# Kernel optimization log

Measured on AMD Instinct MI355X. Metric: run time of the kernel, lower is better.

Reference implementation:

```python
import jax, jax.numpy as jnp
import numpy as np

NUM_GRAPHS = 512  # number of segments (graphs) in the batch
NEG_SLOPE = 0.01  # nn.LeakyReLU default


def setup_inputs() -> dict:
    key = jax.random.key(0)
    k1, k2, k3, k4, k5 = jax.random.split(key, 5)
    N, D = 200000, 128
    h_topo = jax.random.normal(k1, (N, D), dtype=jnp.float32)
    h_geom = jax.random.normal(k2, (N, D), dtype=jnp.float32)
    batch = jnp.sort(jax.random.randint(k3, (N,), 0, NUM_GRAPHS, dtype=jnp.int64))
    concat_dim, hidden, out_dim = 6 * D, 2 * D, 128
    W1 = jax.random.normal(k4, (concat_dim, hidden), dtype=jnp.float32) * 0.02
    b1 = jnp.zeros((hidden,), dtype=jnp.float32)
    W2 = jax.random.normal(k5, (hidden, out_dim), dtype=jnp.float32) * 0.02
    b2 = jnp.zeros((out_dim,), dtype=jnp.float32)
    return {"h_topo": h_topo, "h_geom": h_geom, "batch": batch,
            "W1": W1, "b1": b1, "W2": W2, "b2": b2}


def _pool_feats(h, batch):
    # global_max_pool / global_mean_pool keyed by graph id, gathered back per node
    gmax = jax.ops.segment_max(h, batch, num_segments=NUM_GRAPHS)
    gsum = jax.ops.segment_sum(h, batch, num_segments=NUM_GRAPHS)
    cnt = jax.ops.segment_sum(jnp.ones((h.shape[0],), h.dtype), batch,
                              num_segments=NUM_GRAPHS)
    gmean = gsum / jnp.maximum(cnt, 1.0)[:, None]
    return gmax[batch], gmean[batch]  # [N, D] each


def reference(h_topo, h_geom, batch, W1, b1, W2, b2):
    t_max, t_mean = _pool_feats(h_topo, batch)
    g_max, g_mean = _pool_feats(h_geom, batch)
    # [Topo, Geom, TopoMax, TopoMean, GeomMax, GeomMean]
    combined = jnp.concatenate(
        [h_topo, t_max, t_mean, h_geom, g_max, g_mean], axis=-1)  # [N, 6D]
    h = combined @ W1 + b1
    h = jnp.where(h >= 0, h, NEG_SLOPE * h)  # LeakyReLU
    return h @ W2 + b2
```

## Files before the change

### kernel.cpp

```cpp
#include <hip/hip_runtime.h>
#include <math.h>

#define NUM_GRAPHS 512
#define D 128
#define NEG 0.01f
#define BN 64

typedef __attribute__((ext_vector_type(8))) short  bf16x8;
typedef __attribute__((ext_vector_type(4))) float  f32x4;

__device__ __forceinline__ unsigned short f2bf(float f) {
    unsigned u = __float_as_uint(f);
    u += 0x7fffu + ((u >> 16) & 1u);
    return (unsigned short)(u >> 16);
}

__device__ __forceinline__ uint2 pack4(float4 v) {
    uint2 pk;
    pk.x = (unsigned)f2bf(v.x) | ((unsigned)f2bf(v.y) << 16);
    pk.y = (unsigned)f2bf(v.z) | ((unsigned)f2bf(v.w) << 16);
    return pk;
}

__device__ __forceinline__ int swz(int row, int k) {
    return row * 256 + (k ^ ((row & 7) << 3));
}

#define GLD16(gsrc, ldst)                                                    \
    __builtin_amdgcn_global_load_lds(                                        \
        (const __attribute__((address_space(1))) void*)(gsrc),               \
        (__attribute__((address_space(3))) void*)(ldst), 16, 0, 0)

#define LDS_BARRIER()                                                        \
    do {                                                                     \
        asm volatile("s_waitcnt lgkmcnt(0)" ::: "memory");                   \
        __builtin_amdgcn_s_barrier();                                        \
        asm volatile("" ::: "memory");                                       \
    } while (0)

__global__ __launch_bounds__(256) void pool_kernel(
    const float* __restrict__ h_topo, const float* __restrict__ h_geom,
    const int* __restrict__ batch, int N, float* __restrict__ pooled,
    unsigned short* __restrict__ xt)
{
    const int g = blockIdx.x, t = blockIdx.y;
    const float* __restrict__ h = t ? h_geom : h_topo;
    const int koff = t ? 128 : 0;

    int lo = 0, hi = N;
    while (lo < hi) { int m = (lo + hi) >> 1; if (batch[m] < g) lo = m + 1; else hi = m; }
    const int start = lo; hi = N;
    while (lo < hi) { int m = (lo + hi) >> 1; if (batch[m] < g + 1) lo = m + 1; else hi = m; }
    const int end = lo;

    const int c = threadIdx.x & 31;
    const int r = threadIdx.x >> 5;
    const int kk = koff + c * 4;

    float4 mx  = make_float4(-INFINITY, -INFINITY, -INFINITY, -INFINITY);
    float4 mx2 = mx;
    float4 sm  = make_float4(0.f, 0.f, 0.f, 0.f);
    float4 sm2 = sm;

    int row = start + r;
    for (; row + 8 < end; row += 16) {
        float4 v = *(const float4*)(h + (size_t)row * D + c * 4);
        float4 w = *(const float4*)(h + (size_t)(row + 8) * D + c * 4);
        mx.x  = fmaxf(mx.x,  v.x); mx.y  = fmaxf(mx.y,  v.y);
        mx.z  = fmaxf(mx.z,  v.z); mx.w  = fmaxf(mx.w,  v.w);
        sm.x += v.x; sm.y += v.y; sm.z += v.z; sm.w += v.w;
        mx2.x = fmaxf(mx2.x, w.x); mx2.y = fmaxf(mx2.y, w.y);
        mx2.z = fmaxf(mx2.z, w.z); mx2.w = fmaxf(mx2.w, w.w);
        sm2.x += w.x; sm2.y += w.y; sm2.z += w.z; sm2.w += w.w;
        *(uint2*)(xt + (size_t)(row >> 6) * 16384 + swz(row & 63, kk)) = pack4(v);
        *(uint2*)(xt + (size_t)((row + 8) >> 6) * 16384 + swz((row + 8) & 63, kk)) = pack4(w);
    }
    if (row < end) {
        float4 v = *(const float4*)(h + (size_t)row * D + c * 4);
        mx.x  = fmaxf(mx.x,  v.x); mx.y  = fmaxf(mx.y,  v.y);
        mx.z  = fmaxf(mx.z,  v.z); mx.w  = fmaxf(mx.w,  v.w);
        sm.x += v.x; sm.y += v.y; sm.z += v.z; sm.w += v.w;
        *(uint2*)(xt + (size_t)(row >> 6) * 16384 + swz(row & 63, kk)) = pack4(v);
    }
    mx.x = fmaxf(mx.x, mx2.x); mx.y = fmaxf(mx.y, mx2.y);
    mx.z = fmaxf(mx.z, mx2.z); mx.w = fmaxf(mx.w, mx2.w);
    sm.x += sm2.x; sm.y += sm2.y; sm.z += sm2.z; sm.w += sm2.w;

    __shared__ float4 smx[256], ssm[256];
    smx[threadIdx.x] = mx; ssm[threadIdx.x] = sm;
    __syncthreads();
    #pragma unroll
    for (int s = 4; s > 0; s >>= 1) {
        if (r < s) {
            float4 a = smx[threadIdx.x + s * 32];
            float4 b = ssm[threadIdx.x + s * 32];
            float4 m0 = smx[threadIdx.x];
            float4 s0 = ssm[threadIdx.x];
            m0.x = fmaxf(m0.x, a.x); m0.y = fmaxf(m0.y, a.y);
            m0.z = fmaxf(m0.z, a.z); m0.w = fmaxf(m0.w, a.w);
            s0.x += b.x; s0.y += b.y; s0.z += b.z; s0.w += b.w;
            smx[threadIdx.x] = m0; ssm[threadIdx.x] = s0;
        }
        __syncthreads();
    }
    if (r == 0) {
        float4 m0 = smx[threadIdx.x], s0 = ssm[threadIdx.x];
        const float inv = 1.0f / fmaxf((float)(end - start), 1.0f);
        float4 mean = make_float4(s0.x * inv, s0.y * inv, s0.z * inv, s0.w * inv);
        if (end <= start) { m0 = make_float4(0,0,0,0); mean = make_float4(0,0,0,0); }
        float* dst = pooled + (size_t)g * 512 + t * 256;
        *(float4*)(dst + c * 4)       = m0;
        *(float4*)(dst + 128 + c * 4) = mean;
    }
}

__global__ __launch_bounds__(256) void pmat_kernel(
    const float* __restrict__ pooled, const float* __restrict__ W1,
    const float* __restrict__ b1, float* __restrict__ P)
{
    const int g = blockIdx.x;
    const int j = threadIdx.x;

    __shared__ float pl[512];
    pl[j]       = pooled[(size_t)g * 512 + j];
    pl[j + 256] = pooled[(size_t)g * 512 + 256 + j];
    __syncthreads();

    float acc = b1[j];
    #pragma unroll 8
    for (int k = 0; k < 256; ++k)
        acc += pl[k] * W1[(size_t)(128 + k) * 256 + j];
    #pragma unroll 8
    for (int k = 0; k < 256; ++k)
        acc += pl[256 + k] * W1[(size_t)(512 + k) * 256 + j];

    P[(size_t)g * 256 + j] = acc;
}

__global__ __launch_bounds__(256) void wconv_kernel(
    const float* __restrict__ W1, const float* __restrict__ W2,
    unsigned short* __restrict__ W1bT, unsigned short* __restrict__ W2bT)
{
    const int idx = blockIdx.x * 256 + threadIdx.x;
    if (idx < 256 * 256) {
        const int n = idx >> 8, k = idx & 255;
        const int kk = (k < 128) ? k : (k + 256);
        W1bT[idx] = f2bf(W1[(size_t)kk * 256 + n]);
    } else {
        const int j = idx - 256 * 256;
        if (j < 128 * 256) {
            const int n = j >> 8, k = j & 255;
            W2bT[j] = f2bf(W2[(size_t)k * 128 + n]);
        }
    }
}

__global__ __launch_bounds__(256, 3) void mlp_mfma(
    const unsigned short* __restrict__ xt, const int* __restrict__ batch,
    const float* __restrict__ P,
    const unsigned short* __restrict__ W1bT, const unsigned short* __restrict__ W2bT,
    const float* __restrict__ b2, float* __restrict__ out, int N)
{
    __shared__ unsigned short xs[64 * 256];
    __shared__ int gid[64];

    const int tid  = threadIdx.x;
    const int wave = tid >> 6, lane = tid & 63;
    const int base = blockIdx.x * BN;
    const size_t tbase = (size_t)blockIdx.x * 16384;

    #pragma unroll
    for (int c = 0; c < 8; ++c) {
        const int off = wave * 4096 + c * 512;
        GLD16(xt + tbase + off + lane * 8, xs + off);
    }
    if (tid < 64) gid[tid] = batch[min(base + tid, N - 1)];

    const int g0 = batch[base];
    const int g1 = batch[min(base + 63, N - 1)];
    const bool uni = (g0 == g1);

    const int lhi = lane >> 4;
    const int llo = lane & 15;

    const unsigned short* w1p = W1bT + (size_t)(wave * 64 + llo) * 256 + lhi * 8;
    const unsigned short* w2p = W2bT + (size_t)(wave * 32 + llo) * 256 + lhi * 8;

    float pf[4];
    if (uni) {
        #pragma unroll
        for (int ct = 0; ct < 4; ++ct)
            pf[ct] = P[(size_t)g0 * 256 + wave * 64 + ct * 16 + llo];
    }

    bf16x8 bfr[2][4];
    #pragma unroll
    for (int ct = 0; ct < 4; ++ct)
        bfr[0][ct] = *(const bf16x8*)(w1p + (size_t)ct * 16 * 256);

    asm volatile("s_waitcnt vmcnt(0)" ::: "memory");
    __syncthreads();

    f32x4 acc[4][4];
    #pragma unroll
    for (int rt = 0; rt < 4; ++rt)
        #pragma unroll
        for (int ct = 0; ct < 4; ++ct) {
            const float p = uni ? pf[ct] : 0.f;
            acc[rt][ct] = (f32x4){p, p, p, p};
        }

    #pragma unroll
    for (int ks = 0; ks < 8; ++ks) {
        if (ks < 7) {
            const int kbn = (ks + 1) * 32;
            #pragma unroll
            for (int ct = 0; ct < 4; ++ct)
                bfr[(ks + 1) & 1][ct] = *(const bf16x8*)(w1p + (size_t)ct * 16 * 256 + kbn);
        }
        const int kb = ks * 32 + lhi * 8;
        bf16x8 afr[4];
        #pragma unroll
        for (int rt = 0; rt < 4; ++rt)
            afr[rt] = *(const bf16x8*)&xs[swz(rt * 16 + llo, kb)];
        __builtin_amdgcn_s_setprio(1);
        #pragma unroll
        for (int rt = 0; rt < 4; ++rt)
            #pragma unroll
            for (int ct = 0; ct < 4; ++ct)
                acc[rt][ct] = __builtin_amdgcn_mfma_f32_16x16x32_bf16(
                    afr[rt], bfr[ks & 1][ct], acc[rt][ct], 0, 0, 0);
        __builtin_amdgcn_s_setprio(0);
    }

    bf16x8 bfr2[2][2];
    #pragma unroll
    for (int ct = 0; ct < 2; ++ct)
        bfr2[0][ct] = *(const bf16x8*)(w2p + (size_t)ct * 16 * 256);

    LDS_BARRIER();

    #pragma unroll
    for (int rt = 0; rt < 4; ++rt) {
        #pragma unroll
        for (int ct = 0; ct < 4; ++ct) {
            const int col = wave * 64 + ct * 16 + llo;
            #pragma unroll
            for (int q = 0; q < 4; ++q) {
                const int row = rt * 16 + lhi * 4 + q;
                float v = acc[rt][ct][q];
                if (!uni) v += P[(size_t)gid[row] * 256 + col];
                v = fmaxf(v, NEG * v);
                xs[swz(row, col)] = f2bf(v);
            }
        }
    }

    LDS_BARRIER();

    f32x4 acc2[4][2];
    #pragma unroll
    for (int ct = 0; ct < 2; ++ct) {
        const float bv = b2[wave * 32 + ct * 16 + llo];
        #pragma unroll
        for (int rt = 0; rt < 4; ++rt)
            acc2[rt][ct] = (f32x4){bv, bv, bv, bv};
    }
    #pragma unroll
    for (int ks = 0; ks < 8; ++ks) {
        if (ks < 7) {
            const int kbn = (ks + 1) * 32;
            #pragma unroll
            for (int ct = 0; ct < 2; ++ct)
                bfr2[(ks + 1) & 1][ct] = *(const bf16x8*)(w2p + (size_t)ct * 16 * 256 + kbn);
        }
        const int kb = ks * 32 + lhi * 8;
        bf16x8 afr[4];
        #pragma unroll
        for (int rt = 0; rt < 4; ++rt)
            afr[rt] = *(const bf16x8*)&xs[swz(rt * 16 + llo, kb)];
        __builtin_amdgcn_s_setprio(1);
        #pragma unroll
        for (int rt = 0; rt < 4; ++rt)
            #pragma unroll
            for (int ct = 0; ct < 2; ++ct)
                acc2[rt][ct] = __builtin_amdgcn_mfma_f32_16x16x32_bf16(
                    afr[rt], bfr2[ks & 1][ct], acc2[rt][ct], 0, 0, 0);
        __builtin_amdgcn_s_setprio(0);
    }

    #pragma unroll
    for (int rt = 0; rt < 4; ++rt)
        #pragma unroll
        for (int ct = 0; ct < 2; ++ct)
            #pragma unroll
            for (int q = 0; q < 4; ++q) {
                const int row  = rt * 16 + lhi * 4 + q;
                const int node = base + row;
                if (node < N)
                    out[(size_t)node * 128 + wave * 32 + ct * 16 + llo] = acc2[rt][ct][q];
            }
}

extern "C" void kernel_launch(void* const* d_in, const int* in_sizes, int n_in,
                              void* d_out, int out_size, void* d_ws, size_t ws_size,
                              hipStream_t stream)
{
    const float* h_topo = (const float*)d_in[0];
    const float* h_geom = (const float*)d_in[1];
    const int*   batch  = (const int*)  d_in[2];
    const float* W1     = (const float*)d_in[3];
    const float* b1     = (const float*)d_in[4];
    const float* W2     = (const float*)d_in[5];
    const float* b2     = (const float*)d_in[6];
    float* out = (float*)d_out;

    const int N = in_sizes[0] / D;

    float*          pooled = (float*)d_ws;
    float*          P      = pooled + (size_t)NUM_GRAPHS * 512;
    unsigned short* W1bT   = (unsigned short*)(P + (size_t)NUM_GRAPHS * 256);
    unsigned short* W2bT   = W1bT + 256 * 256;

    const size_t small_bytes = (size_t)(NUM_GRAPHS * 512 + NUM_GRAPHS * 256) * 4
                             + (size_t)(256 * 256 + 128 * 256) * 2;
    const size_t xt_bytes = (size_t)N * 256 * 2;

    unsigned short* xt;
    if (ws_size >= small_bytes + xt_bytes)
        xt = (unsigned short*)((char*)d_ws + small_bytes);
    else
        xt = (unsigned short*)d_out;

    wconv_kernel<<<(256 * 256 + 128 * 256) / 256, 256, 0, stream>>>(W1, W2, W1bT, W2bT);
    pool_kernel<<<dim3(NUM_GRAPHS, 2), 256, 0, stream>>>(h_topo, h_geom, batch, N,
                                                         pooled, xt);
    pmat_kernel<<<NUM_GRAPHS, 256, 0, stream>>>(pooled, W1, b1, P);

    mlp_mfma<<<N / BN, 256, 0, stream>>>(xt, batch, P, W1bT, W2bT, b2, out, N);
}
```

Before: 206.3 us.

## Split per-graph pooling across sub-blocks and deepen weight prefetch in MLP kernel

The pooling kernel now splits each graph's node range into four slices, one block per slice, so the grid grows from 1024 to 4096 blocks and covers the GPU better. Each slice writes a partial max and sum. The pmat kernel recomputes the segment bounds and combines the partials into max and mean. Separately, the MLP kernel prefetches W1 fragments two k-steps ahead and W2 fragments four steps ahead, to hide global load latency, at the cost of more registers.

After: 212.5 us. 1.03x slower.

```diff
diff --git a/kernel.cpp b/kernel.cpp
--- a/kernel.cpp
+++ b/kernel.cpp
@@ -5,6 +5,7 @@
 #define D 128
 #define NEG 0.01f
 #define BN 64
+#define NS 4
 
 typedef __attribute__((ext_vector_type(8))) short  bf16x8;
 typedef __attribute__((ext_vector_type(4))) float  f32x4;
@@ -40,10 +41,10 @@
 
 __global__ __launch_bounds__(256) void pool_kernel(
     const float* __restrict__ h_topo, const float* __restrict__ h_geom,
-    const int* __restrict__ batch, int N, float* __restrict__ pooled,
+    const int* __restrict__ batch, int N, float* __restrict__ pp,
     unsigned short* __restrict__ xt)
 {
-    const int g = blockIdx.x, t = blockIdx.y;
+    const int g = blockIdx.x, t = blockIdx.y, s = blockIdx.z;
     const float* __restrict__ h = t ? h_geom : h_topo;
     const int koff = t ? 128 : 0;
 
@@ -53,6 +54,10 @@
     while (lo < hi) { int m = (lo + hi) >> 1; if (batch[m] < g + 1) lo = m + 1; else hi = m; }
     const int end = lo;
 
+    const int len = end - start;
+    const int r0  = start + (int)(((long long)len * s) / NS);
+    const int r1  = start + (int)(((long long)len * (s + 1)) / NS);
+
     const int c = threadIdx.x & 31;
     const int r = threadIdx.x >> 5;
     const int kk = koff + c * 4;
@@ -62,8 +67,8 @@
     float4 sm  = make_float4(0.f, 0.f, 0.f, 0.f);
     float4 sm2 = sm;
 
-    int row = start + r;
-    for (; row + 8 < end; row += 16) {
+    int row = r0 + r;
+    for (; row + 8 < r1; row += 16) {
         float4 v = *(const float4*)(h + (size_t)row * D + c * 4);
         float4 w = *(const float4*)(h + (size_t)(row + 8) * D + c * 4);
         mx.x  = fmaxf(mx.x,  v.x); mx.y  = fmaxf(mx.y,  v.y);
@@ -75,7 +80,7 @@
         *(uint2*)(xt + (size_t)(row >> 6) * 16384 + swz(row & 63, kk)) = pack4(v);
         *(uint2*)(xt + (size_t)((row + 8) >> 6) * 16384 + swz((row + 8) & 63, kk)) = pack4(w);
     }
-    if (row < end) {
+    if (row < r1) {
         float4 v = *(const float4*)(h + (size_t)row * D + c * 4);
         mx.x  = fmaxf(mx.x,  v.x); mx.y  = fmaxf(mx.y,  v.y);
         mx.z  = fmaxf(mx.z,  v.z); mx.w  = fmaxf(mx.w,  v.w);
@@ -90,10 +95,10 @@
     smx[threadIdx.x] = mx; ssm[threadIdx.x] = sm;
     __syncthreads();
     #pragma unroll
-    for (int s = 4; s > 0; s >>= 1) {
-        if (r < s) {
-            float4 a = smx[threadIdx.x + s * 32];
-            float4 b = ssm[threadIdx.x + s * 32];
+    for (int st = 4; st > 0; st >>= 1) {
+        if (r < st) {
+            float4 a = smx[threadIdx.x + st * 32];
+            float4 b = ssm[threadIdx.x + st * 32];
             float4 m0 = smx[threadIdx.x];
             float4 s0 = ssm[threadIdx.x];
             m0.x = fmaxf(m0.x, a.x); m0.y = fmaxf(m0.y, a.y);
@@ -104,26 +109,41 @@
         __syncthreads();
     }
     if (r == 0) {
-        float4 m0 = smx[threadIdx.x], s0 = ssm[threadIdx.x];
-        const float inv = 1.0f / fmaxf((float)(end - start), 1.0f);
-        float4 mean = make_float4(s0.x * inv, s0.y * inv, s0.z * inv, s0.w * inv);
-        if (end <= start) { m0 = make_float4(0,0,0,0); mean = make_float4(0,0,0,0); }
-        float* dst = pooled + (size_t)g * 512 + t * 256;
-        *(float4*)(dst + c * 4)       = m0;
-        *(float4*)(dst + 128 + c * 4) = mean;
+        float* dst = pp + ((size_t)(g * 2 + t) * NS + s) * 256;
+        *(float4*)(dst + c * 4)       = smx[threadIdx.x];
+        *(float4*)(dst + 128 + c * 4) = ssm[threadIdx.x];
     }
 }
 
 __global__ __launch_bounds__(256) void pmat_kernel(
-    const float* __restrict__ pooled, const float* __restrict__ W1,
-    const float* __restrict__ b1, float* __restrict__ P)
+    const float* __restrict__ pp, const int* __restrict__ batch, int N,
+    const float* __restrict__ W1, const float* __restrict__ b1,
+    float* __restrict__ P)
 {
     const int g = blockIdx.x;
     const int j = threadIdx.x;
 
+    int lo = 0, hi = N;
+    while (lo < hi) { int m = (lo + hi) >> 1; if (batch[m] < g) lo = m + 1; else hi = m; }
+    const int start = lo; hi = N;
+    while (lo < hi) { int m = (lo + hi) >> 1; if (batch[m] < g + 1) lo = m + 1; else hi = m; }
+    const int end = lo;
+    const float inv   = 1.0f / fmaxf((float)(end - start), 1.0f);
+    const bool  empty = (end <= start);
+
     __shared__ float pl[512];
-    pl[j]       = pooled[(size_t)g * 512 + j];
-    pl[j + 256] = pooled[(size_t)g * 512 + 256 + j];
+    #pragma unroll
+    for (int e0 = 0; e0 < 2; ++e0) {
+        const int e = j + e0 * 256;
+        const int t = e >> 8, i = e & 255;
+        const float* q = pp + (size_t)(g * 2 + t) * NS * 256 + i;
+        float v;
+        if (i < 128)
+            v = fmaxf(fmaxf(q[0], q[256]), fmaxf(q[512], q[768]));
+        else
+            v = (q[0] + q[256] + q[512] + q[768]) * inv;
+        pl[e] = empty ? 0.f : v;
+    }
     __syncthreads();
 
     float acc = b1[j];
@@ -195,8 +215,10 @@
 
     bf16x8 bfr[2][4];
     #pragma unroll
-    for (int ct = 0; ct < 4; ++ct)
+    for (int ct = 0; ct < 4; ++ct) {
         bfr[0][ct] = *(const bf16x8*)(w1p + (size_t)ct * 16 * 256);
+        bfr[1][ct] = *(const bf16x8*)(w1p + (size_t)ct * 16 * 256 + 32);
+    }
 
     asm volatile("s_waitcnt vmcnt(0)" ::: "memory");
     __syncthreads();
@@ -212,12 +234,6 @@
 
     #pragma unroll
     for (int ks = 0; ks < 8; ++ks) {
-        if (ks < 7) {
-            const int kbn = (ks + 1) * 32;
-            #pragma unroll
-            for (int ct = 0; ct < 4; ++ct)
-                bfr[(ks + 1) & 1][ct] = *(const bf16x8*)(w1p + (size_t)ct * 16 * 256 + kbn);
-        }
         const int kb = ks * 32 + lhi * 8;
         bf16x8 afr[4];
         #pragma unroll
@@ -231,12 +247,20 @@
                 acc[rt][ct] = __builtin_amdgcn_mfma_f32_16x16x32_bf16(
                     afr[rt], bfr[ks & 1][ct], acc[rt][ct], 0, 0, 0);
         __builtin_amdgcn_s_setprio(0);
-    }
-
-    bf16x8 bfr2[2][2];
-    #pragma unroll
-    for (int ct = 0; ct < 2; ++ct)
-        bfr2[0][ct] = *(const bf16x8*)(w2p + (size_t)ct * 16 * 256);
+        if (ks < 6) {
+            const int kbn = (ks + 2) * 32;
+            #pragma unroll
+            for (int ct = 0; ct < 4; ++ct)
+                bfr[ks & 1][ct] = *(const bf16x8*)(w1p + (size_t)ct * 16 * 256 + kbn);
+        }
+    }
+
+    bf16x8 bfr2[4][2];
+    #pragma unroll
+    for (int k0 = 0; k0 < 4; ++k0)
+        #pragma unroll
+        for (int ct = 0; ct < 2; ++ct)
+            bfr2[k0][ct] = *(const bf16x8*)(w2p + (size_t)ct * 16 * 256 + k0 * 32);
 
     LDS_BARRIER();
 
@@ -268,12 +292,6 @@
     }
     #pragma unroll
     for (int ks = 0; ks < 8; ++ks) {
-        if (ks < 7) {
-            const int kbn = (ks + 1) * 32;
-            #pragma unroll
-            for (int ct = 0; ct < 2; ++ct)
-                bfr2[(ks + 1) & 1][ct] = *(const bf16x8*)(w2p + (size_t)ct * 16 * 256 + kbn);
-        }
         const int kb = ks * 32 + lhi * 8;
         bf16x8 afr[4];
         #pragma unroll
@@ -285,8 +303,14 @@
             #pragma unroll
             for (int ct = 0; ct < 2; ++ct)
                 acc2[rt][ct] = __builtin_amdgcn_mfma_f32_16x16x32_bf16(
-                    afr[rt], bfr2[ks & 1][ct], acc2[rt][ct], 0, 0, 0);
+                    afr[rt], bfr2[ks & 3][ct], acc2[rt][ct], 0, 0, 0);
         __builtin_amdgcn_s_setprio(0);
+        if (ks < 4) {
+            const int kbn = (ks + 4) * 32;
+            #pragma unroll
+            for (int ct = 0; ct < 2; ++ct)
+                bfr2[ks & 3][ct] = *(const bf16x8*)(w2p + (size_t)ct * 16 * 256 + kbn);
+        }
     }
 
     #pragma unroll
@@ -317,12 +341,13 @@
 
     const int N = in_sizes[0] / D;
 
-    float*          pooled = (float*)d_ws;
-    float*          P      = pooled + (size_t)NUM_GRAPHS * 512;
-    unsigned short* W1bT   = (unsigned short*)(P + (size_t)NUM_GRAPHS * 256);
-    unsigned short* W2bT   = W1bT + 256 * 256;
-
-    const size_t small_bytes = (size_t)(NUM_GRAPHS * 512 + NUM_GRAPHS * 256) * 4
+    float*          pp   = (float*)d_ws;
+    float*          P    = pp + (size_t)NUM_GRAPHS * 2 * NS * 256;
+    unsigned short* W1bT = (unsigned short*)(P + (size_t)NUM_GRAPHS * 256);
+    unsigned short* W2bT = W1bT + 256 * 256;
+
+    const size_t small_bytes = (size_t)NUM_GRAPHS * 2 * NS * 256 * 4
+                             + (size_t)NUM_GRAPHS * 256 * 4
                              + (size_t)(256 * 256 + 128 * 256) * 2;
     const size_t xt_bytes = (size_t)N * 256 * 2;
 
@@ -333,9 +358,9 @@
         xt = (unsigned short*)d_out;
 
     wconv_kernel<<<(256 * 256 + 128 * 256) / 256, 256, 0, stream>>>(W1, W2, W1bT, W2bT);
-    pool_kernel<<<dim3(NUM_GRAPHS, 2), 256, 0, stream>>>(h_topo, h_geom, batch, N,
-                                                         pooled, xt);
-    pmat_kernel<<<NUM_GRAPHS, 256, 0, stream>>>(pooled, W1, b1, P);
+    pool_kernel<<<dim3(NUM_GRAPHS, 2, NS), 256, 0, stream>>>(h_topo, h_geom, batch, N,
+                                                             pp, xt);
+    pmat_kernel<<<NUM_GRAPHS, 256, 0, stream>>>(pp, batch, N, W1, b1, P);
 
     mlp_mfma<<<N / BN, 256, 0, stream>>>(xt, batch, P, W1bT, W2bT, b2, out, N);
 }
```
